# Optimization experiments

Hardware: AMD Instinct MI355X
Metric: run time of the kernel (lower is better)

The kernel has to match this reference:

```python
import jax, jax.numpy as jnp
import numpy as np
import math

T, B, E, H = 1024, 4, 512, 8
HD = E // H

def setup_inputs() -> dict:
    key = jax.random.key(0)
    ks = jax.random.split(key, 6)
    return {
        "query": jax.random.normal(ks[0], (T, B, E), dtype=jnp.float32),
        "dist": jax.random.normal(ks[1], (B, T, T, H), dtype=jnp.float32) * 0.1,
        "in_proj_weight": jax.random.normal(ks[2], (3 * E, E), dtype=jnp.float32) * 0.02,
        "in_proj_bias": jax.random.normal(ks[3], (3 * E,), dtype=jnp.float32) * 0.02,
        "out_proj_weight": jax.random.normal(ks[4], (E, E), dtype=jnp.float32) * 0.02,
        "out_proj_bias": jax.random.normal(ks[5], (E,), dtype=jnp.float32) * 0.02,
    }

def reference(query, dist, in_proj_weight, in_proj_bias, out_proj_weight, out_proj_bias):
    t, b, e = query.shape
    # packed in-projection (self-attention: q=k=v=query)
    qkv = query @ in_proj_weight.T + in_proj_bias          # [T,B,3E]
    q, k, v = jnp.split(qkv, 3, axis=-1)                   # each [T,B,E]
    def heads(x):
        return x.reshape(t, b * H, HD).transpose(1, 0, 2)  # [B*H,T,HD]
    q, k, v = heads(q), heads(k), heads(v)
    q = q / math.sqrt(HD)
    attn = jnp.einsum('bte,bse->bts', q, k)                # [B*H,T,T]
    # distance/structure bias: [B,T,T,H] -> [B,H,T,T] -> [B*H,T,T]
    bias = jnp.transpose(dist, (0, 3, 1, 2)).reshape(b * H, t, t)
    attn = jax.nn.softmax(attn + bias, axis=-1)
    out = jnp.einsum('bts,bse->bte', attn, v)              # [B*H,T,HD]
    out = out.transpose(1, 0, 2).reshape(t, b, e)          # [T,B,E]
    out = out @ out_proj_weight.T + out_proj_bias
    return out
```

## Files before the change

kernel.cpp:

```cpp
#include <hip/hip_runtime.h>
#include <math.h>

typedef __bf16 bf16;
typedef bf16 bf16x8 __attribute__((ext_vector_type(8)));
typedef bf16 bf16x4 __attribute__((ext_vector_type(4)));
typedef float f32x4 __attribute__((ext_vector_type(4)));

#define T_DIM 1024
#define B_DIM 4
#define E_DIM 512
#define H_DIM 8
#define HD_DIM 64
#define BH_DIM 32
#define SPLIT 4
#define S_PER (T_DIM / SPLIT)

__device__ __forceinline__ f32x4 mfma16(bf16x8 a, bf16x8 b, f32x4 c) {
    return __builtin_amdgcn_mfma_f32_16x16x32_bf16(a, b, c, 0, 0, 0);
}

__device__ __forceinline__ bf16x4 cvt4(f32x4 v) {
    bf16x4 o;
    o[0] = (bf16)v[0]; o[1] = (bf16)v[1]; o[2] = (bf16)v[2]; o[3] = (bf16)v[3];
    return o;
}

#define CVT_Q_V   524288
#define CVT_W1_V  196608
__global__ __launch_bounds__(256)
void prep(const float* __restrict__ dist, bf16* __restrict__ bias_t,
          const float* __restrict__ q, const float* __restrict__ w1,
          const float* __restrict__ w2, bf16* __restrict__ qo,
          bf16* __restrict__ w1o, bf16* __restrict__ w2o) {
    __shared__ __align__(16) bf16 tile[8 * 1032];
    if (blockIdx.x >= 4096) {
        long v = (long)(blockIdx.x - 4096) * 256 + threadIdx.x;
        const float* src; bf16* dst;
        if (v < CVT_Q_V)                { src = q;  dst = qo; }
        else if (v < CVT_Q_V + CVT_W1_V){ v -= CVT_Q_V;  src = w1; dst = w1o; }
        else                            { v -= CVT_Q_V + CVT_W1_V; src = w2; dst = w2o; }
        f32x4 f = *(const f32x4*)(src + v * 4);
        *(bf16x4*)(dst + v * 4) = cvt4(f);
        return;
    }
    const int bt = blockIdx.x;
    const int b = bt >> 10, t = bt & 1023;
    const int tid = threadIdx.x;
    const float* src = dist + ((long)bt << 13) + tid * 32;
    const int s0 = tid * 4;
    float v[32];
#pragma unroll
    for (int j = 0; j < 8; j++) {
        f32x4 f = *(const f32x4*)(src + j * 4);
        v[j * 4 + 0] = f[0]; v[j * 4 + 1] = f[1];
        v[j * 4 + 2] = f[2]; v[j * 4 + 3] = f[3];
    }
#pragma unroll
    for (int h = 0; h < 8; h++)
#pragma unroll
        for (int si = 0; si < 4; si++)
            tile[h * 1032 + s0 + si] = (bf16)v[si * 8 + h];
    __syncthreads();
#pragma unroll
    for (int rep = 0; rep < 4; rep++) {
        int slot = rep * 256 + tid;
        int h = slot >> 7;
        int sc = (slot & 127) * 8;
        bf16x8 o = *(const bf16x8*)&tile[h * 1032 + sc];
        *(bf16x8*)&bias_t[((long)(b * 8 + h) * T_DIM + t) * T_DIM + sc] = o;
    }
}

template<int TM, int TN, int MODE>
__global__ __launch_bounds__(256)
void gemm_t(const bf16* __restrict__ A, const bf16* __restrict__ Bt,
            const float* __restrict__ bias, int K, int N,
            float* __restrict__ out, bf16* __restrict__ qb,
            bf16* __restrict__ kb, bf16* __restrict__ vb) {
    constexpr int FM = TM / 32, FN = TN / 32;
    constexpr int PA = TM / 64, PB = TN / 64;
    __shared__ __align__(16) bf16 As[2][TM * 72];
    __shared__ __align__(16) bf16 Bs[2][TN * 72];
    const int tid  = threadIdx.x;
    const int lane = tid & 63;
    const int wave = tid >> 6;
    const int quad = lane >> 4;
    const int l15  = lane & 15;
    const int wm = wave & 1, wn = wave >> 1;
    const int m0 = blockIdx.x * TM, n0 = blockIdx.y * TN;

    f32x4 acc[FM][FN] = {};

    const int sr = tid >> 2;
    const int sc = (tid & 3) * 16;

    bf16x8 ra[PA][2], rb[PB][2];
#pragma unroll
    for (int p = 0; p < PA; p++) {
        const bf16* src = &A[(long)(m0 + p * 64 + sr) * K + sc];
        ra[p][0] = *(const bf16x8*)(src);
        ra[p][1] = *(const bf16x8*)(src + 8);
    }
#pragma unroll
    for (int p = 0; p < PB; p++) {
        const bf16* src = &Bt[(long)(n0 + p * 64 + sr) * K + sc];
        rb[p][0] = *(const bf16x8*)(src);
        rb[p][1] = *(const bf16x8*)(src + 8);
    }

    const int NK = K >> 6;
    for (int i = 0; i < NK; i++) {
        const int cur = i & 1;
        bf16* as = As[cur];
        bf16* bs = Bs[cur];
#pragma unroll
        for (int p = 0; p < PA; p++) {
            *(bf16x8*)&as[(p * 64 + sr) * 72 + sc]     = ra[p][0];
            *(bf16x8*)&as[(p * 64 + sr) * 72 + sc + 8] = ra[p][1];
        }
#pragma unroll
        for (int p = 0; p < PB; p++) {
            *(bf16x8*)&bs[(p * 64 + sr) * 72 + sc]     = rb[p][0];
            *(bf16x8*)&bs[(p * 64 + sr) * 72 + sc + 8] = rb[p][1];
        }
        __syncthreads();

        if (i + 1 < NK) {
            const int kn = (i + 1) << 6;
#pragma unroll
            for (int p = 0; p < PA; p++) {
                const bf16* src = &A[(long)(m0 + p * 64 + sr) * K + kn + sc];
                ra[p][0] = *(const bf16x8*)(src);
                ra[p][1] = *(const bf16x8*)(src + 8);
            }
#pragma unroll
            for (int p = 0; p < PB; p++) {
                const bf16* src = &Bt[(long)(n0 + p * 64 + sr) * K + kn + sc];
                rb[p][0] = *(const bf16x8*)(src);
                rb[p][1] = *(const bf16x8*)(src + 8);
            }
        }

#pragma unroll
        for (int kk = 0; kk < 64; kk += 32) {
            bf16x8 af[FM], bfr[FN];
#pragma unroll
            for (int mb = 0; mb < FM; mb++)
                af[mb] = *(const bf16x8*)&as[(wm * (TM / 2) + mb * 16 + l15) * 72 + kk + quad * 8];
#pragma unroll
            for (int nb = 0; nb < FN; nb++)
                bfr[nb] = *(const bf16x8*)&bs[(wn * (TN / 2) + nb * 16 + l15) * 72 + kk + quad * 8];
#pragma unroll
            for (int mb = 0; mb < FM; mb++)
#pragma unroll
                for (int nb = 0; nb < FN; nb++)
                    acc[mb][nb] = mfma16(af[mb], bfr[nb], acc[mb][nb]);
        }
    }

#pragma unroll
    for (int mb = 0; mb < FM; mb++) {
#pragma unroll
        for (int nb = 0; nb < FN; nb++) {
            int n = n0 + wn * (TN / 2) + nb * 16 + l15;
            float bv = bias[n];
#pragma unroll
            for (int r = 0; r < 4; r++) {
                int m = m0 + wm * (TM / 2) + mb * 16 + quad * 4 + r;
                float v = acc[mb][nb][r] + bv;
                if (MODE == 0) {
                    out[(long)m * N + n] = v;
                } else {
                    int t = m >> 2, b = m & 3;
                    int sec = n >> 9, j = n & 511;
                    int h = j >> 6, hd = j & 63;
                    int bh = b * 8 + h;
                    if (sec == 0)
                        qb[((long)bh * T_DIM + t) * HD_DIM + hd] = (bf16)(v * 0.125f);
                    else if (sec == 1)
                        kb[((long)bh * T_DIM + t) * HD_DIM + hd] = (bf16)v;
                    else
                        vb[((long)bh * HD_DIM + hd) * T_DIM + t] = (bf16)v;
                }
            }
        }
    }
}

__global__ __launch_bounds__(256)
void attn_kernel(const bf16* __restrict__ qb, const bf16* __restrict__ kb,
                 const bf16* __restrict__ vb, const bf16* __restrict__ bias_t,
                 float* __restrict__ po, float* __restrict__ pl) {
    __shared__ __align__(16) bf16 Ks[64 * 72];
    __shared__ __align__(16) bf16 Vts[64 * 72];
    __shared__ __align__(16) bf16 Ps[4 * 16 * 72];
    const int tid  = threadIdx.x;
    const int lane = tid & 63;
    const int wave = tid >> 6;
    const int quad = lane >> 4;
    const int l15  = lane & 15;
    const int bid  = blockIdx.x;
    const int bh   = (bid >> 4) & 31;
    const int qt   = bid & 15;
    const int split = bid >> 9;
    const int s0   = split * S_PER;
    const int qrow = qt * 64 + wave * 16 + l15;

    bf16x8 qa0 = *(const bf16x8*)&qb[((long)bh * T_DIM + qrow) * HD_DIM + quad * 8];
    bf16x8 qa1 = *(const bf16x8*)&qb[((long)bh * T_DIM + qrow) * HD_DIM + 32 + quad * 8];

    f32x4 oacc[4] = {};
    float lsum[4] = {0.f, 0.f, 0.f, 0.f};

    const int r0 = tid >> 3;
    const int c0 = (tid & 7) * 8;

    const bf16* dp = bias_t + ((long)bh * T_DIM + qt * 64 + wave * 16 + quad * 4) * T_DIM;

    bf16x8 pk0, pk1, pv0, pv1;
    float pbias[16];
    pk0 = *(const bf16x8*)&kb[((long)bh * T_DIM + s0 + r0) * HD_DIM + c0];
    pk1 = *(const bf16x8*)&kb[((long)bh * T_DIM + s0 + r0 + 32) * HD_DIM + c0];
    pv0 = *(const bf16x8*)&vb[((long)bh * HD_DIM + r0) * T_DIM + s0 + c0];
    pv1 = *(const bf16x8*)&vb[((long)bh * HD_DIM + r0 + 32) * T_DIM + s0 + c0];
#pragma unroll
    for (int r = 0; r < 4; r++)
#pragma unroll
        for (int nb = 0; nb < 4; nb++)
            pbias[r * 4 + nb] = (float)dp[(long)r * T_DIM + s0 + nb * 16 + l15];

    for (int st = s0; st < s0 + S_PER; st += 64) {
        __syncthreads();
        *(bf16x8*)&Ks[r0 * 72 + c0]         = pk0;
        *(bf16x8*)&Ks[(r0 + 32) * 72 + c0]  = pk1;
        *(bf16x8*)&Vts[r0 * 72 + c0]        = pv0;
        *(bf16x8*)&Vts[(r0 + 32) * 72 + c0] = pv1;
        __syncthreads();

        if (st + 64 < s0 + S_PER) {
            const int sn = st + 64;
            pk0 = *(const bf16x8*)&kb[((long)bh * T_DIM + sn + r0) * HD_DIM + c0];
            pk1 = *(const bf16x8*)&kb[((long)bh * T_DIM + sn + r0 + 32) * HD_DIM + c0];
            pv0 = *(const bf16x8*)&vb[((long)bh * HD_DIM + r0) * T_DIM + sn + c0];
            pv1 = *(const bf16x8*)&vb[((long)bh * HD_DIM + r0 + 32) * T_DIM + sn + c0];
        }

        f32x4 sacc[4] = {};
        __builtin_amdgcn_s_setprio(1);
#pragma unroll
        for (int kk = 0; kk < 64; kk += 32) {
            bf16x8 a = (kk == 0) ? qa0 : qa1;
#pragma unroll
            for (int nb = 0; nb < 4; nb++) {
                bf16x8 bfr = *(const bf16x8*)&Ks[(nb * 16 + l15) * 72 + kk + quad * 8];
                sacc[nb] = mfma16(a, bfr, sacc[nb]);
            }
        }
        __builtin_amdgcn_s_setprio(0);

        bf16* pw = &Ps[wave * 16 * 72];
#pragma unroll
        for (int r = 0; r < 4; r++) {
            float rs = 0.f;
#pragma unroll
            for (int nb = 0; nb < 4; nb++) {
                float p = __expf(sacc[nb][r] + pbias[r * 4 + nb]);
                rs += p;
                pw[(quad * 4 + r) * 72 + nb * 16 + l15] = (bf16)p;
            }
            lsum[r] += rs;
        }

        if (st + 64 < s0 + S_PER) {
            const int sn = st + 64;
#pragma unroll
            for (int r = 0; r < 4; r++)
#pragma unroll
                for (int nb = 0; nb < 4; nb++)
                    pbias[r * 4 + nb] = (float)dp[(long)r * T_DIM + sn + nb * 16 + l15];
        }

        __builtin_amdgcn_s_setprio(1);
#pragma unroll
        for (int kk = 0; kk < 64; kk += 32) {
            bf16x8 ap = *(const bf16x8*)&pw[l15 * 72 + kk + quad * 8];
#pragma unroll
            for (int nb = 0; nb < 4; nb++) {
                bf16x8 bv2 = *(const bf16x8*)&Vts[(nb * 16 + l15) * 72 + kk + quad * 8];
                oacc[nb] = mfma16(ap, bv2, oacc[nb]);
            }
        }
        __builtin_amdgcn_s_setprio(0);
    }

#pragma unroll
    for (int r = 0; r < 4; r++) {
#pragma unroll
        for (int msk = 1; msk < 16; msk <<= 1)
            lsum[r] += __shfl_xor(lsum[r], msk);
    }

    float* pob = po + (long)split * (BH_DIM * T_DIM * HD_DIM);
#pragma unroll
    for (int nb = 0; nb < 4; nb++) {
#pragma unroll
        for (int r = 0; r < 4; r++) {
            int t  = qt * 64 + wave * 16 + quad * 4 + r;
            int hd = nb * 16 + l15;
            pob[((long)bh * T_DIM + t) * HD_DIM + hd] = oacc[nb][r];
        }
    }
    if (l15 == 0) {
#pragma unroll
        for (int r = 0; r < 4; r++) {
            int t = qt * 64 + wave * 16 + quad * 4 + r;
            pl[(long)split * (BH_DIM * T_DIM) + bh * T_DIM + t] = lsum[r];
        }
    }
}

__global__ __launch_bounds__(256)
void combine(const float* __restrict__ po, const float* __restrict__ pl,
             bf16* __restrict__ ctxb) {
    const int gid = blockIdx.x * 256 + threadIdx.x;
    const int hd4 = gid & 15;
    const int t   = (gid >> 4) & 1023;
    const int bh  = gid >> 14;
    const long base = ((long)bh * T_DIM + t) * HD_DIM + hd4 * 4;
    f32x4 o = {};
    float l = 0.f;
#pragma unroll
    for (int s = 0; s < SPLIT; s++) {
        o += *(const f32x4*)&po[(long)s * (BH_DIM * T_DIM * HD_DIM) + base];
        l += pl[(long)s * (BH_DIM * T_DIM) + bh * T_DIM + t];
    }
    float inv = 1.f / l;
    f32x4 r = o * inv;
    const int b = bh >> 3, hh = bh & 7;
    *(bf16x4*)&ctxb[((long)t * B_DIM + b) * E_DIM + hh * HD_DIM + hd4 * 4] = cvt4(r);
}

extern "C" void kernel_launch(void* const* d_in, const int* in_sizes, int n_in,
                              void* d_out, int out_size, void* d_ws, size_t ws_size,
                              hipStream_t stream) {
    const float* query = (const float*)d_in[0];
    const float* dist  = (const float*)d_in[1];
    const float* win   = (const float*)d_in[2];
    const float* bin   = (const float*)d_in[3];
    const float* wout  = (const float*)d_in[4];
    const float* bout  = (const float*)d_in[5];
    float* out = (float*)d_out;

    bf16* bias_t = (bf16*)d_ws;
    bf16* qb   = bias_t + ((long)BH_DIM * T_DIM * T_DIM);
    bf16* kb   = qb + (1 << 21);
    bf16* vb   = kb + (1 << 21);
    bf16* qbf  = vb + (1 << 21);
    bf16* w1bf = qbf + (1 << 21);
    bf16* w2bf = w1bf + 786432;
    bf16* ctxb = w2bf + 262144;
    float* po  = (float*)(ctxb + (1 << 21));
    float* pl  = po + (long)SPLIT * BH_DIM * T_DIM * HD_DIM;

    prep<<<dim3(7168), 256, 0, stream>>>(dist, bias_t, query, win, wout,
                                         qbf, w1bf, w2bf);
    gemm_t<64, 192, 1><<<dim3(64, 8), 256, 0, stream>>>(
        qbf, w1bf, bin, 512, 1536, nullptr, qb, kb, vb);
    attn_kernel<<<dim3(512 * SPLIT), 256, 0, stream>>>(qb, kb, vb, bias_t, po, pl);
    combine<<<dim3(2048), 256, 0, stream>>>(po, pl, ctxb);
    gemm_t<64, 64, 0><<<dim3(64, 8), 256, 0, stream>>>(
        ctxb, w2bf, bout, 512, 512, out, nullptr, nullptr, nullptr);
}
```

Measured before the change: 277.7 us.

## Remove split-KV in attention and normalize output directly in kernel

Drops the 4-way split over the key dimension, so each attention block loops over all 1024 keys and writes the normalized bf16 context straight into the out-projection input. The separate combine kernel and its fp32 partial-output traffic go away, along with one launch. In exchange the attention grid shrinks from 2048 to 512 blocks, which lowers parallelism and occupancy on a GPU with many CUs, and each block's loop becomes four times longer.

```diff
diff --git a/kernel.cpp b/kernel.cpp
--- a/kernel.cpp
+++ b/kernel.cpp
@@ -12,8 +12,6 @@
 #define H_DIM 8
 #define HD_DIM 64
 #define BH_DIM 32
-#define SPLIT 4
-#define S_PER (T_DIM / SPLIT)
 
 __device__ __forceinline__ f32x4 mfma16(bf16x8 a, bf16x8 b, f32x4 c) {
     return __builtin_amdgcn_mfma_f32_16x16x32_bf16(a, b, c, 0, 0, 0);
@@ -190,7 +188,7 @@
 __global__ __launch_bounds__(256)
 void attn_kernel(const bf16* __restrict__ qb, const bf16* __restrict__ kb,
                  const bf16* __restrict__ vb, const bf16* __restrict__ bias_t,
-                 float* __restrict__ po, float* __restrict__ pl) {
+                 bf16* __restrict__ ctxb) {
     __shared__ __align__(16) bf16 Ks[64 * 72];
     __shared__ __align__(16) bf16 Vts[64 * 72];
     __shared__ __align__(16) bf16 Ps[4 * 16 * 72];
@@ -200,10 +198,9 @@
     const int quad = lane >> 4;
     const int l15  = lane & 15;
     const int bid  = blockIdx.x;
-    const int bh   = (bid >> 4) & 31;
+    const int bh   = bid >> 4;
     const int qt   = bid & 15;
-    const int split = bid >> 9;
-    const int s0   = split * S_PER;
+    const int b    = bh >> 3, h = bh & 7;
     const int qrow = qt * 64 + wave * 16 + l15;
 
     bf16x8 qa0 = *(const bf16x8*)&qb[((long)bh * T_DIM + qrow) * HD_DIM + quad * 8];
@@ -219,17 +216,17 @@
 
     bf16x8 pk0, pk1, pv0, pv1;
     float pbias[16];
-    pk0 = *(const bf16x8*)&kb[((long)bh * T_DIM + s0 + r0) * HD_DIM + c0];
-    pk1 = *(const bf16x8*)&kb[((long)bh * T_DIM + s0 + r0 + 32) * HD_DIM + c0];
-    pv0 = *(const bf16x8*)&vb[((long)bh * HD_DIM + r0) * T_DIM + s0 + c0];
-    pv1 = *(const bf16x8*)&vb[((long)bh * HD_DIM + r0 + 32) * T_DIM + s0 + c0];
+    pk0 = *(const bf16x8*)&kb[((long)bh * T_DIM + r0) * HD_DIM + c0];
+    pk1 = *(const bf16x8*)&kb[((long)bh * T_DIM + r0 + 32) * HD_DIM + c0];
+    pv0 = *(const bf16x8*)&vb[((long)bh * HD_DIM + r0) * T_DIM + c0];
+    pv1 = *(const bf16x8*)&vb[((long)bh * HD_DIM + r0 + 32) * T_DIM + c0];
 #pragma unroll
     for (int r = 0; r < 4; r++)
 #pragma unroll
         for (int nb = 0; nb < 4; nb++)
-            pbias[r * 4 + nb] = (float)dp[(long)r * T_DIM + s0 + nb * 16 + l15];
-
-    for (int st = s0; st < s0 + S_PER; st += 64) {
+            pbias[r * 4 + nb] = (float)dp[(long)r * T_DIM + nb * 16 + l15];
+
+    for (int st = 0; st < T_DIM; st += 64) {
         __syncthreads();
         *(bf16x8*)&Ks[r0 * 72 + c0]         = pk0;
         *(bf16x8*)&Ks[(r0 + 32) * 72 + c0]  = pk1;
@@ -237,7 +234,7 @@
         *(bf16x8*)&Vts[(r0 + 32) * 72 + c0] = pv1;
         __syncthreads();
 
-        if (st + 64 < s0 + S_PER) {
+        if (st + 64 < T_DIM) {
             const int sn = st + 64;
             pk0 = *(const bf16x8*)&kb[((long)bh * T_DIM + sn + r0) * HD_DIM + c0];
             pk1 = *(const bf16x8*)&kb[((long)bh * T_DIM + sn + r0 + 32) * HD_DIM + c0];
@@ -271,7 +268,7 @@
             lsum[r] += rs;
         }
 
-        if (st + 64 < s0 + S_PER) {
+        if (st + 64 < T_DIM) {
             const int sn = st + 64;
 #pragma unroll
             for (int r = 0; r < 4; r++)
@@ -300,44 +297,16 @@
             lsum[r] += __shfl_xor(lsum[r], msk);
     }
 
-    float* pob = po + (long)split * (BH_DIM * T_DIM * HD_DIM);
 #pragma unroll
     for (int nb = 0; nb < 4; nb++) {
 #pragma unroll
         for (int r = 0; r < 4; r++) {
             int t  = qt * 64 + wave * 16 + quad * 4 + r;
             int hd = nb * 16 + l15;
-            pob[((long)bh * T_DIM + t) * HD_DIM + hd] = oacc[nb][r];
-        }
-    }
-    if (l15 == 0) {
-#pragma unroll
-        for (int r = 0; r < 4; r++) {
-            int t = qt * 64 + wave * 16 + quad * 4 + r;
-            pl[(long)split * (BH_DIM * T_DIM) + bh * T_DIM + t] = lsum[r];
-        }
-    }
-}
-
-__global__ __launch_bounds__(256)
-void combine(const float* __restrict__ po, const float* __restrict__ pl,
-             bf16* __restrict__ ctxb) {
-    const int gid = blockIdx.x * 256 + threadIdx.x;
-    const int hd4 = gid & 15;
-    const int t   = (gid >> 4) & 1023;
-    const int bh  = gid >> 14;
-    const long base = ((long)bh * T_DIM + t) * HD_DIM + hd4 * 4;
-    f32x4 o = {};
-    float l = 0.f;
-#pragma unroll
-    for (int s = 0; s < SPLIT; s++) {
-        o += *(const f32x4*)&po[(long)s * (BH_DIM * T_DIM * HD_DIM) + base];
-        l += pl[(long)s * (BH_DIM * T_DIM) + bh * T_DIM + t];
-    }
-    float inv = 1.f / l;
-    f32x4 r = o * inv;
-    const int b = bh >> 3, hh = bh & 7;
-    *(bf16x4*)&ctxb[((long)t * B_DIM + b) * E_DIM + hh * HD_DIM + hd4 * 4] = cvt4(r);
+            float o = oacc[nb][r] / lsum[r];
+            ctxb[((long)t * B_DIM + b) * E_DIM + h * HD_DIM + hd] = (bf16)o;
+        }
+    }
 }
 
 extern "C" void kernel_launch(void* const* d_in, const int* in_sizes, int n_in,
@@ -359,15 +328,12 @@
     bf16* w1bf = qbf + (1 << 21);
     bf16* w2bf = w1bf + 786432;
     bf16* ctxb = w2bf + 262144;
-    float* po  = (float*)(ctxb + (1 << 21));
-    float* pl  = po + (long)SPLIT * BH_DIM * T_DIM * HD_DIM;
 
     prep<<<dim3(7168), 256, 0, stream>>>(dist, bias_t, query, win, wout,
                                          qbf, w1bf, w2bf);
     gemm_t<64, 192, 1><<<dim3(64, 8), 256, 0, stream>>>(
         qbf, w1bf, bin, 512, 1536, nullptr, qb, kb, vb);
-    attn_kernel<<<dim3(512 * SPLIT), 256, 0, stream>>>(qb, kb, vb, bias_t, po, pl);
-    combine<<<dim3(2048), 256, 0, stream>>>(po, pl, ctxb);
+    attn_kernel<<<dim3(512), 256, 0, stream>>>(qb, kb, vb, bias_t, ctxb);
     gemm_t<64, 64, 0><<<dim3(64, 8), 256, 0, stream>>>(
         ctxb, w2bf, bout, 512, 512, out, nullptr, nullptr, nullptr);
 }
```

Result: faster. 268.1 us (-3.5%).
